# Kernel optimization log

Hardware: AMD Instinct MI355X
Metric: run time of the kernel (lower is better)

Reference implementation:

```python
import jax, jax.numpy as jnp
import numpy as np

NUM_VARIABLES = 20
NUM_LAYERS = 3
NUM_CONSTRAINTS = 64
NUM_STATES = 2 ** NUM_VARIABLES
TOP_K = 10  # min(10, num_states)


def _state_bits():
    # bits[i, v] = v-th bit of i, MSB first (matches format(i, '0{n}b'))
    idx = jnp.arange(NUM_STATES, dtype=jnp.int32)
    shifts = jnp.arange(NUM_VARIABLES - 1, -1, -1, dtype=jnp.int32)
    return ((idx[:, None] >> shifts[None, :]) & 1).astype(jnp.float32)


def setup_inputs() -> dict:
    key = jax.random.key(0)
    k1, k2, k3 = jax.random.split(key, 3)
    return {
        "problem_constraints": jax.random.normal(k1, (NUM_CONSTRAINTS, NUM_VARIABLES), dtype=jnp.float32),
        "beta_params": jax.random.normal(k2, (NUM_LAYERS,), dtype=jnp.float32) * 0.1,
        "gamma_params": jax.random.normal(k3, (NUM_LAYERS,), dtype=jnp.float32) * 0.1,
    }


def reference(problem_constraints, beta_params, gamma_params):
    bits = _state_bits()  # [S, n]
    # cost_function evaluated on every basis state (vectorized over 2^n states)
    viol = bits @ problem_constraints.T  # [S, C]
    costs = jnp.sum(jnp.maximum(viol - 1.0, 0.0) ** 2, axis=1) + 0.1 * jnp.sum(bits, axis=1)
    costs = jax.lax.stop_gradient(costs)  # torch fills costs via .item(), detaching them

    amps = jnp.full((NUM_STATES,), 1.0 / np.sqrt(NUM_STATES), dtype=jnp.float32)
    for layer in range(NUM_LAYERS):
        # problem unitary: exp(-i*gamma*cost) applied to real amps, then cast back
        # to float32 (torch .to(float) keeps the real part) => multiply by cos.
        amps = amps * jnp.cos(gamma_params[layer] * costs)
        # mixer: mixed[i] = amps[i] + 0.1*sin(beta) * sum_bit amps[i ^ (1<<bit)]
        grid = amps.reshape((2,) * NUM_VARIABLES)
        nb = jnp.zeros_like(grid)
        for ax in range(NUM_VARIABLES):  # structural loop over qubit axes
            nb = nb + jnp.flip(grid, axis=ax)
        mixed = amps + 0.1 * jnp.sin(beta_params[layer]) * nb.reshape(-1)
        amps = mixed / jnp.linalg.norm(mixed)

    probs = amps ** 2  # |amplitude|^2 (amps are real after the casts)
    _, top_idx = jax.lax.top_k(probs, TOP_K)
    top_assignments = bits[top_idx]  # [K, n]
    assignment_costs = costs[top_idx]  # same formula as cost_function on each
    best = jnp.argmin(assignment_costs)
    optimal_assignment = top_assignments[best]
    optimal_cost = assignment_costs[best]
    return (optimal_assignment, optimal_cost, probs, top_assignments, assignment_costs)
```

## Files before the change

kernel.cpp:

```cpp
#include <hip/hip_runtime.h>
#include <math.h>

#define NV 20
#define NC 64
#define NSTATES (1u << 20)
#define TOPK 10
#define NB1 256
#define NCAND (NB1 * TOPK)

__device__ __forceinline__ unsigned dbswz(unsigned x) {
    return ((x & 7u) << 5) | (x >> 3);
}

__global__ __launch_bounds__(512) void k_costs(const float* __restrict__ C,
                                               float* __restrict__ costs,
                                               float* __restrict__ ph0,
                                               const float* __restrict__ gamma,
                                               double* __restrict__ scal,
                                               unsigned* __restrict__ ctr) {
    __shared__ float CT[17][NC];
    __shared__ float lowT[8][NC];
    const int tid = threadIdx.x;

    if (blockIdx.x == 0) {
        if (tid < 8) scal[tid] = 0.0;
        if (tid == 8) *ctr = 0u;
    }

    for (int e = tid; e < 17 * NC; e += 512) {
        int k = e / NC, c = e % NC;
        CT[k][c] = C[c * NV + (16 - k)];
    }
    for (int e = tid; e < 8 * NC; e += 512) {
        int m = e >> 6, c = e & 63;
        float v = 0.0f;
        if (m & 1) v += C[c * NV + 19];
        if (m & 2) v += C[c * NV + 18];
        if (m & 4) v += C[c * NV + 17];
        lowT[m][c] = v;
    }
    __syncthreads();

    const unsigned db = dbswz(blockIdx.x);
    unsigned t = db * 512u + (unsigned)tid;
    float g0 = gamma[0];

    float cost[8];
    #pragma unroll
    for (int s = 0; s < 8; ++s)
        cost[s] = 0.1f * (float)__popc(t * 8u + (unsigned)s);

    #pragma unroll
    for (int cc = 0; cc < 4; ++cc) {
        float4 bb[4];
        #pragma unroll
        for (int q = 0; q < 4; ++q) bb[q] = make_float4(-1.f, -1.f, -1.f, -1.f);
        #pragma unroll
        for (int k = 0; k < 17; ++k) {
            float bf = (float)((t >> k) & 1u);
            const float4* row = ((const float4*)(&CT[k][0])) + 4 * cc;
            #pragma unroll
            for (int q = 0; q < 4; ++q) {
                float4 cv = row[q];
                bb[q].x = fmaf(bf, cv.x, bb[q].x);
                bb[q].y = fmaf(bf, cv.y, bb[q].y);
                bb[q].z = fmaf(bf, cv.z, bb[q].z);
                bb[q].w = fmaf(bf, cv.w, bb[q].w);
            }
        }
        #pragma unroll
        for (int s = 0; s < 8; ++s) {
            const float4* lrow = ((const float4*)(&lowT[s][0])) + 4 * cc;
            #pragma unroll
            for (int q = 0; q < 4; ++q) {
                float4 lv = lrow[q];
                float4 v;
                v.x = bb[q].x + lv.x; v.y = bb[q].y + lv.y;
                v.z = bb[q].z + lv.z; v.w = bb[q].w + lv.w;
                float r;
                r = fmaxf(v.x, 0.f); cost[s] = fmaf(r, r, cost[s]);
                r = fmaxf(v.y, 0.f); cost[s] = fmaf(r, r, cost[s]);
                r = fmaxf(v.z, 0.f); cost[s] = fmaf(r, r, cost[s]);
                r = fmaxf(v.w, 0.f); cost[s] = fmaf(r, r, cost[s]);
            }
        }
    }

    float4* co = (float4*)(costs + (size_t)t * 8u);
    co[0] = make_float4(cost[0], cost[1], cost[2], cost[3]);
    co[1] = make_float4(cost[4], cost[5], cost[6], cost[7]);
    float ph[8];
    #pragma unroll
    for (int s = 0; s < 8; ++s) ph[s] = 0x1p-10f * cosf(g0 * cost[s]);
    float4* po = (float4*)(ph0 + (size_t)t * 8u);
    po[0] = make_float4(ph[0], ph[1], ph[2], ph[3]);
    po[1] = make_float4(ph[4], ph[5], ph[6], ph[7]);
}

template <int LAYER, bool ALIN, bool ALOUT>
__global__ __launch_bounds__(1024, 4) void k_mix(const float* __restrict__ pin,
                                                 const float* __restrict__ costs,
                                                 float* __restrict__ pout,
                                                 const float* __restrict__ gamma,
                                                 const float* __restrict__ beta,
                                                 double* __restrict__ scal) {
    __shared__ float4 tile[1024];
    __shared__ double dpart[16];
    const unsigned lq = threadIdx.x;
    const unsigned db = dbswz(blockIdx.x);
    const unsigned i4 = db * 1024u + lq;
    float s = 0.1f * sinf(beta[LAYER]);
    float prevscale = (LAYER == 0) ? 1.0f : (float)(1.0 / sqrt(scal[LAYER - 1]));

    auto ld4 = [&](unsigned j4) -> float4 {
        if (ALIN) return ((const float4*)pin)[j4];
        float4 a;
        a.x = pin[4u * j4 + 0]; a.y = pin[4u * j4 + 1];
        a.z = pin[4u * j4 + 2]; a.w = pin[4u * j4 + 3];
        return a;
    };

    float4 own = ld4(i4);
    tile[lq] = own;

    float4 gv[8];
    #pragma unroll
    for (int p = 19; p >= 12; --p) gv[19 - p] = ld4(i4 ^ (1u << (p - 2)));

    __syncthreads();

    float4 nb = make_float4(0.f, 0.f, 0.f, 0.f);
    #pragma unroll
    for (int u = 0; u < 8; ++u) {
        nb.x += gv[u].x; nb.y += gv[u].y; nb.z += gv[u].z; nb.w += gv[u].w;
    }
    #pragma unroll
    for (int p = 11; p >= 2; --p) {
        float4 v = tile[lq ^ (1u << (p - 2))];
        nb.x += v.x; nb.y += v.y; nb.z += v.z; nb.w += v.w;
    }
    nb.x += own.z; nb.y += own.w; nb.z += own.x; nb.w += own.y;
    nb.x += own.y; nb.y += own.x; nb.z += own.w; nb.w += own.z;

    float4 m;
    m.x = prevscale * fmaf(s, nb.x, own.x);
    m.y = prevscale * fmaf(s, nb.y, own.y);
    m.z = prevscale * fmaf(s, nb.z, own.z);
    m.w = prevscale * fmaf(s, nb.w, own.w);

    float4 o;
    if (LAYER < 2) {
        float gn = gamma[LAYER + 1];
        float4 c = ((const float4*)costs)[i4];
        o.x = m.x * cosf(gn * c.x);
        o.y = m.y * cosf(gn * c.y);
        o.z = m.z * cosf(gn * c.z);
        o.w = m.w * cosf(gn * c.w);
    } else {
        o = m;
    }
    if (ALOUT) {
        ((float4*)pout)[i4] = o;
    } else {
        pout[4u * i4 + 0] = o.x; pout[4u * i4 + 1] = o.y;
        pout[4u * i4 + 2] = o.z; pout[4u * i4 + 3] = o.w;
    }

    double ss = (double)m.x * m.x + (double)m.y * m.y +
                (double)m.z * m.z + (double)m.w * m.w;
    #pragma unroll
    for (int off = 32; off > 0; off >>= 1) ss += __shfl_down(ss, off);
    int wid = threadIdx.x >> 6;
    if ((threadIdx.x & 63) == 0) dpart[wid] = ss;
    __syncthreads();
    if (threadIdx.x == 0) {
        double tt = 0.0;
        #pragma unroll
        for (int w = 0; w < 16; ++w) tt += dpart[w];
        atomicAdd(&scal[LAYER], tt);
    }
}

template <bool ALIN>
__global__ __launch_bounds__(256) void k_ptop(const float* __restrict__ A,
                                              const double* __restrict__ scal2,
                                              const float* __restrict__ costs,
                                              float* __restrict__ out,
                                              unsigned long long* __restrict__ cand,
                                              unsigned* __restrict__ ctr) {
    __shared__ unsigned long long warr[4];
    __shared__ int lastblk;
    __shared__ unsigned topi[TOPK];
    __shared__ float topc[TOPK];
    const int tid = threadIdx.x;
    float* probs_out = out + 21;
    unsigned b4 = dbswz(blockIdx.x) * 1024u;
    float scale = (float)(1.0 / sqrt(*scal2));

    unsigned long long k[16];
    #pragma unroll
    for (int u = 0; u < 4; ++u) {
        unsigned j4 = b4 + (unsigned)tid + 256u * u;
        float4 v;
        if (ALIN) v = ((const float4*)A)[j4];
        else {
            v.x = A[4u * j4 + 0]; v.y = A[4u * j4 + 1];
            v.z = A[4u * j4 + 2]; v.w = A[4u * j4 + 3];
        }
        float4 p;
        p.x = v.x * scale; p.x *= p.x;
        p.y = v.y * scale; p.y *= p.y;
        p.z = v.z * scale; p.z *= p.z;
        p.w = v.w * scale; p.w *= p.w;
        unsigned e0 = 4u * j4;
        probs_out[e0 + 0] = p.x; probs_out[e0 + 1] = p.y;
        probs_out[e0 + 2] = p.z; probs_out[e0 + 3] = p.w;
        k[4 * u + 0] = ((unsigned long long)__float_as_uint(p.x) << 32) | (unsigned long long)(0xFFFFFFFFu - (e0 + 0));
        k[4 * u + 1] = ((unsigned long long)__float_as_uint(p.y) << 32) | (unsigned long long)(0xFFFFFFFFu - (e0 + 1));
        k[4 * u + 2] = ((unsigned long long)__float_as_uint(p.z) << 32) | (unsigned long long)(0xFFFFFFFFu - (e0 + 2));
        k[4 * u + 3] = ((unsigned long long)__float_as_uint(p.w) << 32) | (unsigned long long)(0xFFFFFFFFu - (e0 + 3));
    }

    for (int r = 0; r < TOPK; ++r) {
        unsigned long long loc = 0ull;
        #pragma unroll
        for (int j = 0; j < 16; ++j) if (k[j] > loc) loc = k[j];
        #pragma unroll
        for (int off = 32; off > 0; off >>= 1) {
            unsigned long long o = __shfl_down(loc, off);
            if (o > loc) loc = o;
        }
        if ((tid & 63) == 0) warr[tid >> 6] = loc;
        __syncthreads();
        unsigned long long win = warr[0];
        if (warr[1] > win) win = warr[1];
        if (warr[2] > win) win = warr[2];
        if (warr[3] > win) win = warr[3];
        __syncthreads();
        #pragma unroll
        for (int j = 0; j < 16; ++j) if (k[j] == win) k[j] = 0ull;
        if (tid == 0) cand[blockIdx.x * TOPK + r] = win;
    }

    __threadfence();
    if (tid == 0) {
        unsigned old = atomicAdd(ctr, 1u);
        lastblk = (old == NB1 - 1) ? 1 : 0;
    }
    __syncthreads();
    if (!lastblk) return;
    __threadfence();

    unsigned long long c2[TOPK];
    #pragma unroll
    for (int u = 0; u < TOPK; ++u) c2[u] = cand[tid + 256 * u];

    for (int r = 0; r < TOPK; ++r) {
        unsigned long long loc = 0ull;
        #pragma unroll
        for (int u = 0; u < TOPK; ++u) if (c2[u] > loc) loc = c2[u];
        #pragma unroll
        for (int off = 32; off > 0; off >>= 1) {
            unsigned long long o = __shfl_down(loc, off);
            if (o > loc) loc = o;
        }
        if ((tid & 63) == 0) warr[tid >> 6] = loc;
        __syncthreads();
        unsigned long long win = warr[0];
        if (warr[1] > win) win = warr[1];
        if (warr[2] > win) win = warr[2];
        if (warr[3] > win) win = warr[3];
        __syncthreads();
        #pragma unroll
        for (int u = 0; u < TOPK; ++u) if (c2[u] == win) c2[u] = 0ull;
        if (tid == 0) topi[r] = 0xFFFFFFFFu - (unsigned)(win & 0xFFFFFFFFull);
        __syncthreads();
    }

    const unsigned S = NSTATES;
    if (tid < TOPK * NV) {
        int kk = tid / NV, vv = tid % NV;
        out[21 + S + (unsigned)tid] = (float)((topi[kk] >> (NV - 1 - vv)) & 1u);
    }
    if (tid < TOPK) {
        float c = costs[topi[tid]];
        topc[tid] = c;
        out[21 + S + TOPK * NV + (unsigned)tid] = c;
    }
    __syncthreads();
    if (tid == 0) {
        int best = 0;
        for (int kk = 1; kk < TOPK; ++kk)
            if (topc[kk] < topc[best]) best = kk;
        unsigned gi = topi[best];
        for (int vv = 0; vv < NV; ++vv)
            out[vv] = (float)((gi >> (NV - 1 - vv)) & 1u);
        out[NV] = topc[best];
    }
}

extern "C" void kernel_launch(void* const* d_in, const int* in_sizes, int n_in,
                              void* d_out_, int out_size, void* d_ws, size_t ws_size,
                              hipStream_t stream) {
    (void)in_sizes; (void)n_in; (void)out_size;
    const float* C     = (const float*)d_in[0];
    const float* beta  = (const float*)d_in[1];
    const float* gamma = (const float*)d_in[2];
    float* out = (float*)d_out_;
    char* ws = (char*)d_ws;
    const size_t S4 = (size_t)NSTATES * sizeof(float);

    double* scal = (double*)ws;
    unsigned* ctr = (unsigned*)(ws + 64);
    unsigned long long* cand = (unsigned long long*)(ws + 1024);
    float* costs = (float*)(ws + 32768);
    float* A     = (float*)(ws + 32768 + S4);
    const size_t need_full = 32768 + 3 * S4;
    bool wsbig = (ws_size >= need_full);
    float* B = wsbig ? (float*)(ws + 32768 + 2 * S4) : (out + 21);

    k_costs<<<256, 512, 0, stream>>>(C, costs, A, gamma, scal, ctr);

    if (wsbig) {
        k_mix<0, true, true ><<<256, 1024, 0, stream>>>(A, costs, B, gamma, beta, scal);
        k_mix<1, true, true ><<<256, 1024, 0, stream>>>(B, costs, A, gamma, beta, scal);
        k_mix<2, true, true ><<<256, 1024, 0, stream>>>(A, costs, B, gamma, beta, scal);
        k_ptop<true ><<<NB1, 256, 0, stream>>>(B, scal + 2, costs, out, cand, ctr);
    } else {
        k_mix<0, true, false><<<256, 1024, 0, stream>>>(A, costs, B, gamma, beta, scal);
        k_mix<1, false, true><<<256, 1024, 0, stream>>>(B, costs, A, gamma, beta, scal);
        k_mix<2, true, false><<<256, 1024, 0, stream>>>(A, costs, B, gamma, beta, scal);
        k_ptop<false><<<NB1, 256, 0, stream>>>(B, scal + 2, costs, out, cand, ctr);
    }
}
```

Before: 89.55 us.

## Store half-precision shadow copies of amplitudes for remote-neighbor gathers in mixer

Each layer now also writes an fp16 copy of the amplitude vector. The mixer reads its 8 high-bit neighbor gathers from that copy, so those loads move half as many bytes, while the block's own values and the in-tile neighbors stay fp32. The block-index swizzle is also dropped in favor of linear block mapping. The cost is extra writes for the half copies and fp16 rounding error in part of the neighbor sum, which could change the top-k ordering among near-tied probabilities.

```diff
diff --git a/kernel.cpp b/kernel.cpp
--- a/kernel.cpp
+++ b/kernel.cpp
@@ -1,4 +1,5 @@
 #include <hip/hip_runtime.h>
+#include <hip/hip_fp16.h>
 #include <math.h>
 
 #define NV 20
@@ -8,13 +9,13 @@
 #define NB1 256
 #define NCAND (NB1 * TOPK)
 
-__device__ __forceinline__ unsigned dbswz(unsigned x) {
-    return ((x & 7u) << 5) | (x >> 3);
-}
-
+struct h4 { __half2 lo, hi; };
+
+template <bool WRITEH>
 __global__ __launch_bounds__(512) void k_costs(const float* __restrict__ C,
                                                float* __restrict__ costs,
                                                float* __restrict__ ph0,
+                                               h4* __restrict__ ph0h,
                                                const float* __restrict__ gamma,
                                                double* __restrict__ scal,
                                                unsigned* __restrict__ ctr) {
@@ -41,8 +42,7 @@
     }
     __syncthreads();
 
-    const unsigned db = dbswz(blockIdx.x);
-    unsigned t = db * 512u + (unsigned)tid;
+    unsigned t = blockIdx.x * 512u + (unsigned)tid;
     float g0 = gamma[0];
 
     float cost[8];
@@ -95,6 +95,95 @@
     float4* po = (float4*)(ph0 + (size_t)t * 8u);
     po[0] = make_float4(ph[0], ph[1], ph[2], ph[3]);
     po[1] = make_float4(ph[4], ph[5], ph[6], ph[7]);
+    if (WRITEH) {
+        h4 h0, h1;
+        h0.lo = __floats2half2_rn(ph[0], ph[1]);
+        h0.hi = __floats2half2_rn(ph[2], ph[3]);
+        h1.lo = __floats2half2_rn(ph[4], ph[5]);
+        h1.hi = __floats2half2_rn(ph[6], ph[7]);
+        ph0h[(size_t)t * 2u + 0] = h0;
+        ph0h[(size_t)t * 2u + 1] = h1;
+    }
+}
+
+template <int LAYER>
+__global__ __launch_bounds__(1024, 4) void k_mixh(const float* __restrict__ pin,
+                                                  const h4* __restrict__ pinh,
+                                                  const float* __restrict__ costs,
+                                                  float* __restrict__ pout,
+                                                  h4* __restrict__ pouth,
+                                                  const float* __restrict__ gamma,
+                                                  const float* __restrict__ beta,
+                                                  double* __restrict__ scal) {
+    __shared__ float4 tile[1024];
+    __shared__ double dpart[16];
+    const unsigned lq = threadIdx.x;
+    const unsigned i4 = blockIdx.x * 1024u + lq;
+    float s = 0.1f * sinf(beta[LAYER]);
+    float prevscale = (LAYER == 0) ? 1.0f : (float)(1.0 / sqrt(scal[LAYER - 1]));
+
+    float4 own = ((const float4*)pin)[i4];
+    tile[lq] = own;
+
+    h4 gv[8];
+    #pragma unroll
+    for (int p = 19; p >= 12; --p) gv[19 - p] = pinh[i4 ^ (1u << (p - 2))];
+
+    __syncthreads();
+
+    float4 nb = make_float4(0.f, 0.f, 0.f, 0.f);
+    #pragma unroll
+    for (int u = 0; u < 8; ++u) {
+        float2 f0 = __half22float2(gv[u].lo);
+        float2 f1 = __half22float2(gv[u].hi);
+        nb.x += f0.x; nb.y += f0.y; nb.z += f1.x; nb.w += f1.y;
+    }
+    #pragma unroll
+    for (int p = 11; p >= 2; --p) {
+        float4 v = tile[lq ^ (1u << (p - 2))];
+        nb.x += v.x; nb.y += v.y; nb.z += v.z; nb.w += v.w;
+    }
+    nb.x += own.z; nb.y += own.w; nb.z += own.x; nb.w += own.y;
+    nb.x += own.y; nb.y += own.x; nb.z += own.w; nb.w += own.z;
+
+    float4 m;
+    m.x = prevscale * fmaf(s, nb.x, own.x);
+    m.y = prevscale * fmaf(s, nb.y, own.y);
+    m.z = prevscale * fmaf(s, nb.z, own.z);
+    m.w = prevscale * fmaf(s, nb.w, own.w);
+
+    float4 o;
+    if (LAYER < 2) {
+        float gn = gamma[LAYER + 1];
+        float4 c = ((const float4*)costs)[i4];
+        o.x = m.x * cosf(gn * c.x);
+        o.y = m.y * cosf(gn * c.y);
+        o.z = m.z * cosf(gn * c.z);
+        o.w = m.w * cosf(gn * c.w);
+    } else {
+        o = m;
+    }
+    ((float4*)pout)[i4] = o;
+    if (LAYER < 2) {
+        h4 oh;
+        oh.lo = __floats2half2_rn(o.x, o.y);
+        oh.hi = __floats2half2_rn(o.z, o.w);
+        pouth[i4] = oh;
+    }
+
+    double ss = (double)m.x * m.x + (double)m.y * m.y +
+                (double)m.z * m.z + (double)m.w * m.w;
+    #pragma unroll
+    for (int off = 32; off > 0; off >>= 1) ss += __shfl_down(ss, off);
+    int wid = threadIdx.x >> 6;
+    if ((threadIdx.x & 63) == 0) dpart[wid] = ss;
+    __syncthreads();
+    if (threadIdx.x == 0) {
+        double tt = 0.0;
+        #pragma unroll
+        for (int w = 0; w < 16; ++w) tt += dpart[w];
+        atomicAdd(&scal[LAYER], tt);
+    }
 }
 
 template <int LAYER, bool ALIN, bool ALOUT>
@@ -107,11 +196,9 @@
     __shared__ float4 tile[1024];
     __shared__ double dpart[16];
     const unsigned lq = threadIdx.x;
-    const unsigned db = dbswz(blockIdx.x);
-    const unsigned i4 = db * 1024u + lq;
+    const unsigned i4 = blockIdx.x * 1024u + lq;
     float s = 0.1f * sinf(beta[LAYER]);
     float prevscale = (LAYER == 0) ? 1.0f : (float)(1.0 / sqrt(scal[LAYER - 1]));
-
     auto ld4 = [&](unsigned j4) -> float4 {
         if (ALIN) return ((const float4*)pin)[j4];
         float4 a;
@@ -119,21 +206,15 @@
         a.z = pin[4u * j4 + 2]; a.w = pin[4u * j4 + 3];
         return a;
     };
-
     float4 own = ld4(i4);
     tile[lq] = own;
-
     float4 gv[8];
     #pragma unroll
     for (int p = 19; p >= 12; --p) gv[19 - p] = ld4(i4 ^ (1u << (p - 2)));
-
-    __syncthreads();
-
+    __syncthreads();
     float4 nb = make_float4(0.f, 0.f, 0.f, 0.f);
     #pragma unroll
-    for (int u = 0; u < 8; ++u) {
-        nb.x += gv[u].x; nb.y += gv[u].y; nb.z += gv[u].z; nb.w += gv[u].w;
-    }
+    for (int u = 0; u < 8; ++u) { nb.x += gv[u].x; nb.y += gv[u].y; nb.z += gv[u].z; nb.w += gv[u].w; }
     #pragma unroll
     for (int p = 11; p >= 2; --p) {
         float4 v = tile[lq ^ (1u << (p - 2))];
@@ -141,33 +222,24 @@
     }
     nb.x += own.z; nb.y += own.w; nb.z += own.x; nb.w += own.y;
     nb.x += own.y; nb.y += own.x; nb.z += own.w; nb.w += own.z;
-
     float4 m;
     m.x = prevscale * fmaf(s, nb.x, own.x);
     m.y = prevscale * fmaf(s, nb.y, own.y);
     m.z = prevscale * fmaf(s, nb.z, own.z);
     m.w = prevscale * fmaf(s, nb.w, own.w);
-
     float4 o;
     if (LAYER < 2) {
         float gn = gamma[LAYER + 1];
         float4 c = ((const float4*)costs)[i4];
-        o.x = m.x * cosf(gn * c.x);
-        o.y = m.y * cosf(gn * c.y);
-        o.z = m.z * cosf(gn * c.z);
-        o.w = m.w * cosf(gn * c.w);
-    } else {
-        o = m;
-    }
-    if (ALOUT) {
-        ((float4*)pout)[i4] = o;
-    } else {
+        o.x = m.x * cosf(gn * c.x); o.y = m.y * cosf(gn * c.y);
+        o.z = m.z * cosf(gn * c.z); o.w = m.w * cosf(gn * c.w);
+    } else o = m;
+    if (ALOUT) ((float4*)pout)[i4] = o;
+    else {
         pout[4u * i4 + 0] = o.x; pout[4u * i4 + 1] = o.y;
         pout[4u * i4 + 2] = o.z; pout[4u * i4 + 3] = o.w;
     }
-
-    double ss = (double)m.x * m.x + (double)m.y * m.y +
-                (double)m.z * m.z + (double)m.w * m.w;
+    double ss = (double)m.x * m.x + (double)m.y * m.y + (double)m.z * m.z + (double)m.w * m.w;
     #pragma unroll
     for (int off = 32; off > 0; off >>= 1) ss += __shfl_down(ss, off);
     int wid = threadIdx.x >> 6;
@@ -194,7 +266,7 @@
     __shared__ float topc[TOPK];
     const int tid = threadIdx.x;
     float* probs_out = out + 21;
-    unsigned b4 = dbswz(blockIdx.x) * 1024u;
+    unsigned b4 = blockIdx.x * 1024u;
     float scale = (float)(1.0 / sqrt(*scal2));
 
     unsigned long long k[16];
@@ -309,27 +381,40 @@
     float* out = (float*)d_out_;
     char* ws = (char*)d_ws;
     const size_t S4 = (size_t)NSTATES * sizeof(float);
+    const size_t S2 = (size_t)NSTATES * 2;
 
     double* scal = (double*)ws;
     unsigned* ctr = (unsigned*)(ws + 64);
     unsigned long long* cand = (unsigned long long*)(ws + 1024);
     float* costs = (float*)(ws + 32768);
     float* A     = (float*)(ws + 32768 + S4);
-    const size_t need_full = 32768 + 3 * S4;
-    bool wsbig = (ws_size >= need_full);
-    float* B = wsbig ? (float*)(ws + 32768 + 2 * S4) : (out + 21);
-
-    k_costs<<<256, 512, 0, stream>>>(C, costs, A, gamma, scal, ctr);
-
-    if (wsbig) {
-        k_mix<0, true, true ><<<256, 1024, 0, stream>>>(A, costs, B, gamma, beta, scal);
-        k_mix<1, true, true ><<<256, 1024, 0, stream>>>(B, costs, A, gamma, beta, scal);
-        k_mix<2, true, true ><<<256, 1024, 0, stream>>>(A, costs, B, gamma, beta, scal);
-        k_ptop<true ><<<NB1, 256, 0, stream>>>(B, scal + 2, costs, out, cand, ctr);
+    float* B     = (float*)(ws + 32768 + 2 * S4);
+    h4*    Ah    = (h4*)(ws + 32768 + 3 * S4);
+    h4*    Bh    = (h4*)(ws + 32768 + 3 * S4 + S2);
+
+    const size_t need_half = 32768 + 3 * S4 + 2 * S2;
+    const size_t need_f32  = 32768 + 3 * S4;
+
+    if (ws_size >= need_half) {
+        k_costs<true><<<256, 512, 0, stream>>>(C, costs, A, Ah, gamma, scal, ctr);
+        k_mixh<0><<<256, 1024, 0, stream>>>(A, Ah, costs, B, Bh, gamma, beta, scal);
+        k_mixh<1><<<256, 1024, 0, stream>>>(B, Bh, costs, A, Ah, gamma, beta, scal);
+        k_mixh<2><<<256, 1024, 0, stream>>>(A, Ah, costs, B, nullptr, gamma, beta, scal);
+        k_ptop<true><<<NB1, 256, 0, stream>>>(B, scal + 2, costs, out, cand, ctr);
     } else {
-        k_mix<0, true, false><<<256, 1024, 0, stream>>>(A, costs, B, gamma, beta, scal);
-        k_mix<1, false, true><<<256, 1024, 0, stream>>>(B, costs, A, gamma, beta, scal);
-        k_mix<2, true, false><<<256, 1024, 0, stream>>>(A, costs, B, gamma, beta, scal);
-        k_ptop<false><<<NB1, 256, 0, stream>>>(B, scal + 2, costs, out, cand, ctr);
+        bool wsbig = (ws_size >= need_f32);
+        float* Bf = wsbig ? B : (out + 21);
+        k_costs<false><<<256, 512, 0, stream>>>(C, costs, A, nullptr, gamma, scal, ctr);
+        if (wsbig) {
+            k_mix<0, true, true ><<<256, 1024, 0, stream>>>(A, costs, Bf, gamma, beta, scal);
+            k_mix<1, true, true ><<<256, 1024, 0, stream>>>(Bf, costs, A, gamma, beta, scal);
+            k_mix<2, true, true ><<<256, 1024, 0, stream>>>(A, costs, Bf, gamma, beta, scal);
+            k_ptop<true ><<<NB1, 256, 0, stream>>>(Bf, scal + 2, costs, out, cand, ctr);
+        } else {
+            k_mix<0, true, false><<<256, 1024, 0, stream>>>(A, costs, Bf, gamma, beta, scal);
+            k_mix<1, false, true><<<256, 1024, 0, stream>>>(Bf, costs, A, gamma, beta, scal);
+            k_mix<2, true, false><<<256, 1024, 0, stream>>>(A, costs, Bf, gamma, beta, scal);
+            k_ptop<false><<<NB1, 256, 0, stream>>>(Bf, scal + 2, costs, out, cand, ctr);
+        }
     }
 }
```

New measurement: 84.66 us, median of 2. 1.06x faster.
